# Kernel tuning notes

Measured on AMD Instinct MI355X. Metric: run time of the kernel, lower is better.

Reference implementation:

```python
import jax, jax.numpy as jnp
import numpy as np

NEG_SLOPE = 0.2

def gatv2(x, edge_index, Wl, bl, Wr, br, att, bias):
    # PyG GATv2Conv (share_weights=False, add_self_loops=True, concat=True)
    N = x.shape[0]
    H, D = att.shape
    src0, dst0 = edge_index[0], edge_index[1]
    # remove_self_loops + add_self_loops semantics: mask existing self loops,
    # append one self loop per node (keeps static shapes under jit)
    loop = jnp.arange(N, dtype=src0.dtype)
    src = jnp.concatenate([src0, loop])
    dst = jnp.concatenate([dst0, loop])
    keep = jnp.concatenate([src0 != dst0, jnp.ones(N, dtype=bool)])  # drop original i->i edges
    xl = (x @ Wl + bl).reshape(N, H, D)  # source-side transform
    xr = (x @ Wr + br).reshape(N, H, D)  # target-side transform
    e = xl[src] + xr[dst]                                  # [E,H,D]
    logits = jnp.einsum('ehd,hd->eh', jax.nn.leaky_relu(e, NEG_SLOPE), att)
    logits = jnp.where(keep[:, None], logits, -jnp.inf)
    m = jax.ops.segment_max(logits, dst, num_segments=N)   # [N,H]
    ex = jnp.where(keep[:, None], jnp.exp(logits - m[dst]), 0.0)
    denom = jax.ops.segment_sum(ex, dst, num_segments=N)   # [N,H]
    alpha = ex / (denom[dst] + 1e-16)                      # [E,H]
    out = jax.ops.segment_sum(alpha[..., None] * xl[src], dst, num_segments=N)
    return out.reshape(N, H * D) + bias

def setup_inputs() -> dict:
    key = jax.random.key(0)
    ks = jax.random.split(key, 20)
    N, E, F, Hd = 50000, 400000, 5, 128
    s = 0.05
    inp = {
        'x': jax.random.normal(ks[0], (N, F), dtype=jnp.float32),
        'edge_index': jax.random.randint(ks[1], (2, E), 0, N, dtype=jnp.int64),
        # node_embed MLP
        'W1': jax.random.normal(ks[2], (F, Hd), dtype=jnp.float32) * s,
        'b1': jnp.zeros((Hd,), jnp.float32),
        'W2': jax.random.normal(ks[3], (Hd, Hd), dtype=jnp.float32) * s,
        'b2': jnp.zeros((Hd,), jnp.float32),
        # gnn1: GATv2Conv(128 -> 128, heads=4)
        'Wl1': jax.random.normal(ks[4], (Hd, 4 * Hd), dtype=jnp.float32) * s,
        'bl1': jnp.zeros((4 * Hd,), jnp.float32),
        'Wr1': jax.random.normal(ks[5], (Hd, 4 * Hd), dtype=jnp.float32) * s,
        'br1': jnp.zeros((4 * Hd,), jnp.float32),
        'att1': jax.random.normal(ks[6], (4, Hd), dtype=jnp.float32) * s,
        'bias1': jnp.zeros((4 * Hd,), jnp.float32),
        # gnn2: GATv2Conv(512 -> 128, heads=1)
        'Wl2': jax.random.normal(ks[7], (4 * Hd, Hd), dtype=jnp.float32) * s,
        'bl2': jnp.zeros((Hd,), jnp.float32),
        'Wr2': jax.random.normal(ks[8], (4 * Hd, Hd), dtype=jnp.float32) * s,
        'br2': jnp.zeros((Hd,), jnp.float32),
        'att2': jax.random.normal(ks[9], (1, Hd), dtype=jnp.float32) * s,
        'bias2': jnp.zeros((Hd,), jnp.float32),
    }
    return inp

def reference(x, edge_index, W1, b1, W2, b2, Wl1, bl1, Wr1, br1, att1, bias1,
              Wl2, bl2, Wr2, br2, att2, bias2):
    h = jax.nn.relu(x @ W1 + b1) @ W2 + b2                 # node_embed MLP
    h = jax.nn.relu(gatv2(h, edge_index, Wl1, bl1, Wr1, br1, att1, bias1))
    out = gatv2(h, edge_index, Wl2, bl2, Wr2, br2, att2, bias2)
    return out  # [N, 128]
```

## Files before the change

### kernel.cpp

```cpp
#include <hip/hip_runtime.h>
#include <math.h>

typedef __attribute__((ext_vector_type(8))) short bf16x8;
typedef __attribute__((ext_vector_type(4))) float f32x4;
typedef unsigned short ushort;

static __device__ __forceinline__ ushort f2bf(float f) {
    unsigned u = __float_as_uint(f);
    u = u + 0x7fff + ((u >> 16) & 1);
    return (ushort)(u >> 16);
}
static __device__ __forceinline__ float bf2f(ushort h) {
    return __uint_as_float(((unsigned)h) << 16);
}


__global__ void k_init(int* __restrict__ counts, int N) {
    int i = blockIdx.x * blockDim.x + threadIdx.x;
    if (i < N) counts[i] = 1;
}

__global__ void k_count(const int* __restrict__ src, const int* __restrict__ dst,
                        int E, int* __restrict__ counts) {
    int e = blockIdx.x * blockDim.x + threadIdx.x;
    if (e < E) {
        int s = src[e], d = dst[e];
        if (s != d) atomicAdd(&counts[d], 1);
    }
}

__global__ __launch_bounds__(256) void k_blocksum(const int* __restrict__ counts, int N,
                                                  int* __restrict__ bsum) {
    __shared__ int s[256];
    int t = threadIdx.x, i = blockIdx.x * 256 + t;
    s[t] = (i < N) ? counts[i] : 0;
    __syncthreads();
    for (int off = 128; off > 0; off >>= 1) {
        if (t < off) s[t] += s[t + off];
        __syncthreads();
    }
    if (t == 0) bsum[blockIdx.x] = s[0];
}

__global__ __launch_bounds__(256) void k_scanblocks(const int* __restrict__ bsum, int NB,
                                                    int* __restrict__ boff,
                                                    int* __restrict__ rowptr, int N) {
    __shared__ int s[256];
    int t = threadIdx.x;
    int v = (t < NB) ? bsum[t] : 0;
    s[t] = v;
    __syncthreads();
    for (int off = 1; off < 256; off <<= 1) {
        int u = (t >= off) ? s[t - off] : 0;
        __syncthreads();
        s[t] += u;
        __syncthreads();
    }
    if (t < NB) boff[t] = s[t] - v;
    if (t == NB - 1) rowptr[N] = s[t];
}

__global__ __launch_bounds__(256) void k_scatter(const int* __restrict__ counts, int N,
                                                 const int* __restrict__ boff,
                                                 int* __restrict__ rowptr,
                                                 int* __restrict__ cursor) {
    __shared__ int s[256];
    int t = threadIdx.x, i = blockIdx.x * 256 + t;
    int c = (i < N) ? counts[i] : 0;
    s[t] = c;
    __syncthreads();
    for (int off = 1; off < 256; off <<= 1) {
        int u = (t >= off) ? s[t - off] : 0;
        __syncthreads();
        s[t] += u;
        __syncthreads();
    }
    if (i < N) {
        int excl = boff[blockIdx.x] + s[t] - c;
        rowptr[i] = excl;
        cursor[i] = excl;
    }
}

__global__ void k_fill(const int* __restrict__ src, const int* __restrict__ dst,
                       int E, int N, int* __restrict__ cursor, int* __restrict__ colA) {
    int i = blockIdx.x * blockDim.x + threadIdx.x;
    if (i < E) {
        int s = src[i], d = dst[i];
        if (s != d) { int p = atomicAdd(&cursor[d], 1); colA[p] = s; }
    } else if (i < E + N) {
        int n = i - E;
        int p = atomicAdd(&cursor[n], 1); colA[p] = n;
    }
}


__global__ __launch_bounds__(256) void k_repack(
    const float* __restrict__ W2, const float* __restrict__ Wl1,
    const float* __restrict__ Wr1, const float* __restrict__ Wl2,
    const float* __restrict__ Wr2,
    ushort* __restrict__ wfh, ushort* __restrict__ wfl)
{
    int job = blockIdx.y;
    int t = blockIdx.x * 256 + threadIdx.x;
    int ks = t >> 9, n = (t >> 6) & 7, l = t & 63;

    const float* W; int ldw, rowoff, col0;
    if (job == 0)      { W = W2;  ldw = 128; rowoff = 0;              col0 = 0; }
    else if (job < 5)  { W = Wl1; ldw = 512; rowoff = 0;              col0 = (job - 1) * 128; }
    else if (job < 9)  { W = Wr1; ldw = 512; rowoff = 0;              col0 = (job - 5) * 128; }
    else if (job < 13) { W = Wl2; ldw = 128; rowoff = (job - 9) * 128;  col0 = 0; }
    else               { W = Wr2; ldw = 128; rowoff = (job - 13) * 128; col0 = 0; }

    int krow = rowoff + ks * 32 + (l >> 4) * 8;
    int col = col0 + n * 16 + (l & 15);
    size_t dbase = (size_t)job * 16384 + (((size_t)(ks * 8 + n)) * 64 + l) * 8;
#pragma unroll
    for (int j = 0; j < 8; j++) {
        float v = W[(size_t)(krow + j) * ldw + col];
        ushort h = f2bf(v);
        ushort lo = f2bf(v - bf2f(h));
        wfh[dbase + j] = h;
        wfl[dbase + j] = lo;
    }
}


__global__ __launch_bounds__(256) void k_mlp1(
    const float* __restrict__ x, const float* __restrict__ W1, const float* __restrict__ b1,
    ushort* __restrict__ outh, ushort* __restrict__ outl, int N)
{
    int n = blockIdx.x * 2 + (threadIdx.x >> 7);
    int j = threadIdx.x & 127;
    if (n >= N) return;
    float s = b1[j];
#pragma unroll
    for (int k = 0; k < 5; k++) s = fmaf(x[(size_t)n * 5 + k], W1[k * 128 + j], s);
    s = fmaxf(s, 0.f);
    ushort h = f2bf(s);
    outh[(size_t)n * 128 + j] = h;
    outl[(size_t)n * 128 + j] = f2bf(s - bf2f(h));
}


__global__ __launch_bounds__(256) void gemm_mfma(
    const ushort* __restrict__ Ah, const ushort* __restrict__ Al,
    const ushort* __restrict__ wfh, const ushort* __restrict__ wfl,
    const float* __restrict__ bias,
    ushort* __restrict__ Ch, ushort* __restrict__ Cl,
    int M)
{
    int tid = threadIdx.x;
    int w = tid >> 6, l = tid & 63;
    int m0 = blockIdx.x * 128 + w * 32;
    int lr = l & 15, kg = l >> 4;

    f32x4 acc[2][8];
#pragma unroll
    for (int i = 0; i < 2; i++)
#pragma unroll
        for (int j = 0; j < 8; j++) acc[i][j] = (f32x4){0.f, 0.f, 0.f, 0.f};

    int row0 = m0 + lr, row1 = m0 + 16 + lr;
    bool ok0 = row0 < M, ok1 = row1 < M;
    const bf16x8 zz = {0, 0, 0, 0, 0, 0, 0, 0};

#pragma unroll
    for (int ks = 0; ks < 4; ks++) {
        int koff = ks * 32 + kg * 8;
        bf16x8 a0h = ok0 ? *(const bf16x8*)(Ah + (size_t)row0 * 128 + koff) : zz;
        bf16x8 a0l = ok0 ? *(const bf16x8*)(Al + (size_t)row0 * 128 + koff) : zz;
        bf16x8 a1h = ok1 ? *(const bf16x8*)(Ah + (size_t)row1 * 128 + koff) : zz;
        bf16x8 a1l = ok1 ? *(const bf16x8*)(Al + (size_t)row1 * 128 + koff) : zz;
#pragma unroll
        for (int n = 0; n < 8; n++) {
            size_t bo = (((size_t)(ks * 8 + n)) * 64 + l) * 8;
            bf16x8 bh = *(const bf16x8*)(wfh + bo);
            bf16x8 bl = *(const bf16x8*)(wfl + bo);
            acc[0][n] = __builtin_amdgcn_mfma_f32_16x16x32_bf16(a0h, bh, acc[0][n], 0, 0, 0);
            acc[0][n] = __builtin_amdgcn_mfma_f32_16x16x32_bf16(a0h, bl, acc[0][n], 0, 0, 0);
            acc[0][n] = __builtin_amdgcn_mfma_f32_16x16x32_bf16(a0l, bh, acc[0][n], 0, 0, 0);
            acc[1][n] = __builtin_amdgcn_mfma_f32_16x16x32_bf16(a1h, bh, acc[1][n], 0, 0, 0);
            acc[1][n] = __builtin_amdgcn_mfma_f32_16x16x32_bf16(a1h, bl, acc[1][n], 0, 0, 0);
            acc[1][n] = __builtin_amdgcn_mfma_f32_16x16x32_bf16(a1l, bh, acc[1][n], 0, 0, 0);
        }
    }

#pragma unroll
    for (int mf = 0; mf < 2; mf++) {
#pragma unroll
        for (int r = 0; r < 4; r++) {
            int row = m0 + mf * 16 + kg * 4 + r;
            if (row >= M) continue;
#pragma unroll
            for (int n = 0; n < 8; n++) {
                size_t idx = (size_t)row * 128 + n * 16 + lr;
                float v = acc[mf][n][r] + bias[n * 16 + lr];
                ushort h = f2bf(v);
                Ch[idx] = h;
                Cl[idx] = f2bf(v - bf2f(h));
            }
        }
    }
}


__global__ __launch_bounds__(256) void gemm_xlr1(
    const ushort* __restrict__ Ah, const ushort* __restrict__ Al,
    const ushort* __restrict__ wh, const ushort* __restrict__ wl,
    const float* __restrict__ bl1, const float* __restrict__ br1,
    ushort* __restrict__ out, int M)
{
    __shared__ __align__(16) ushort Bh[16384];
    __shared__ __align__(16) ushort Bl[16384];

    int tid = threadIdx.x;
    int w = tid >> 6, l = tid & 63;
    int m0 = blockIdx.x * 128 + w * 32;
    int lr = l & 15, kg = l >> 4;

    int row0 = m0 + lr, row1 = m0 + 16 + lr;
    bool ok0 = row0 < M, ok1 = row1 < M;
    const bf16x8 zz = {0, 0, 0, 0, 0, 0, 0, 0};

    bf16x8 a0h[4], a0l[4], a1h[4], a1l[4];
#pragma unroll
    for (int ks = 0; ks < 4; ks++) {
        int koff = ks * 32 + kg * 8;
        a0h[ks] = ok0 ? *(const bf16x8*)(Ah + (size_t)row0 * 128 + koff) : zz;
        a0l[ks] = ok0 ? *(const bf16x8*)(Al + (size_t)row0 * 128 + koff) : zz;
        a1h[ks] = ok1 ? *(const bf16x8*)(Ah + (size_t)row1 * 128 + koff) : zz;
        a1l[ks] = ok1 ? *(const bf16x8*)(Al + (size_t)row1 * 128 + koff) : zz;
    }

    for (int t = 0; t < 8; t++) {
        __syncthreads();
        {
            const float4* gh = (const float4*)(wh + (size_t)t * 16384);
            const float4* gl = (const float4*)(wl + (size_t)t * 16384);
            float4* sh = (float4*)Bh;
            float4* sl = (float4*)Bl;
#pragma unroll
            for (int i = 0; i < 8; i++) {
                sh[i * 256 + tid] = gh[i * 256 + tid];
                sl[i * 256 + tid] = gl[i * 256 + tid];
            }
        }
        __syncthreads();

        f32x4 acc[2][8];
#pragma unroll
        for (int i = 0; i < 2; i++)
#pragma unroll
            for (int j = 0; j < 8; j++) acc[i][j] = (f32x4){0.f, 0.f, 0.f, 0.f};

#pragma unroll
        for (int ks = 0; ks < 4; ks++) {
#pragma unroll
            for (int n = 0; n < 8; n++) {
                int bo = ((ks * 8 + n) * 64 + l) * 8;
                bf16x8 bh = *(const bf16x8*)(Bh + bo);
                bf16x8 bl = *(const bf16x8*)(Bl + bo);
                acc[0][n] = __builtin_amdgcn_mfma_f32_16x16x32_bf16(a0h[ks], bh, acc[0][n], 0, 0, 0);
                acc[0][n] = __builtin_amdgcn_mfma_f32_16x16x32_bf16(a0h[ks], bl, acc[0][n], 0, 0, 0);
                acc[0][n] = __builtin_amdgcn_mfma_f32_16x16x32_bf16(a0l[ks], bh, acc[0][n], 0, 0, 0);
                acc[1][n] = __builtin_amdgcn_mfma_f32_16x16x32_bf16(a1h[ks], bh, acc[1][n], 0, 0, 0);
                acc[1][n] = __builtin_amdgcn_mfma_f32_16x16x32_bf16(a1h[ks], bl, acc[1][n], 0, 0, 0);
                acc[1][n] = __builtin_amdgcn_mfma_f32_16x16x32_bf16(a1l[ks], bh, acc[1][n], 0, 0, 0);
            }
        }

        float bcol[8];
#pragma unroll
        for (int n = 0; n < 8; n++)
            bcol[n] = (t < 4) ? bl1[t * 128 + n * 16 + lr] : br1[(t - 4) * 128 + n * 16 + lr];

#pragma unroll
        for (int mf = 0; mf < 2; mf++) {
#pragma unroll
            for (int r = 0; r < 4; r++) {
                int row = m0 + mf * 16 + kg * 4 + r;
                if (row >= M) continue;
#pragma unroll
                for (int n = 0; n < 8; n++)
                    out[(size_t)row * 1024 + t * 128 + n * 16 + lr] = f2bf(acc[mf][n][r] + bcol[n]);
            }
        }
    }
}


__global__ __launch_bounds__(256) void gemm_xlr2(
    const ushort* __restrict__ A,
    const ushort* __restrict__ wfh, const ushort* __restrict__ wfl,
    const float* __restrict__ bl2, const float* __restrict__ br2,
    ushort* __restrict__ xl2, ushort* __restrict__ xr2, int M)
{
    __shared__ __align__(16) ushort Bh[16384];
    __shared__ __align__(16) ushort Bl[16384];

    int tid = threadIdx.x;
    int w = tid >> 6, l = tid & 63;
    int m0 = blockIdx.x * 64 + w * 16;
    int lr = l & 15, kg = l >> 4;

    int row0 = m0 + lr;
    bool ok0 = row0 < M;
    const bf16x8 zz = {0, 0, 0, 0, 0, 0, 0, 0};

    f32x4 acc[2][8];
#pragma unroll
    for (int i = 0; i < 2; i++)
#pragma unroll
        for (int j = 0; j < 8; j++) acc[i][j] = (f32x4){0.f, 0.f, 0.f, 0.f};

    for (int kc = 0; kc < 4; kc++) {
        bf16x8 ah[4];
#pragma unroll
        for (int ks = 0; ks < 4; ks++)
            ah[ks] = ok0 ? *(const bf16x8*)(A + (size_t)row0 * 512 + kc * 128 + ks * 32 + kg * 8) : zz;

        for (int t = 0; t < 2; t++) {
            int slot = 9 + t * 4 + kc;
            __syncthreads();
            {
                const float4* gh = (const float4*)(wfh + (size_t)slot * 16384);
                const float4* gl = (const float4*)(wfl + (size_t)slot * 16384);
                float4* sh = (float4*)Bh;
                float4* sl = (float4*)Bl;
#pragma unroll
                for (int i = 0; i < 8; i++) {
                    sh[i * 256 + tid] = gh[i * 256 + tid];
                    sl[i * 256 + tid] = gl[i * 256 + tid];
                }
            }
            __syncthreads();
#pragma unroll
            for (int ks = 0; ks < 4; ks++) {
#pragma unroll
                for (int n = 0; n < 8; n++) {
                    int bo = ((ks * 8 + n) * 64 + l) * 8;
                    bf16x8 bh = *(const bf16x8*)(Bh + bo);
                    bf16x8 bl = *(const bf16x8*)(Bl + bo);
                    acc[t][n] = __builtin_amdgcn_mfma_f32_16x16x32_bf16(ah[ks], bh, acc[t][n], 0, 0, 0);
                    acc[t][n] = __builtin_amdgcn_mfma_f32_16x16x32_bf16(ah[ks], bl, acc[t][n], 0, 0, 0);
                }
            }
        }
    }

#pragma unroll
    for (int r = 0; r < 4; r++) {
        int row = m0 + kg * 4 + r;
        if (row >= M) continue;
#pragma unroll
        for (int n = 0; n < 8; n++) {
            int col = n * 16 + lr;
            xl2[(size_t)row * 128 + col] = f2bf(acc[0][n][r] + bl2[col]);
            xr2[(size_t)row * 128 + col] = f2bf(acc[1][n][r] + br2[col]);
        }
    }
}


__global__ __launch_bounds__(256) void gat_edge4(
    const ushort* __restrict__ xlr,
    const float* __restrict__ att,
    const float* __restrict__ bias,
    const int* __restrict__ rowptr, const int* __restrict__ colA,
    ushort* __restrict__ h1,
    int N)
{
    int n = blockIdx.x;
    int h = threadIdx.x >> 6, l = threadIdx.x & 63;
    int g = l >> 4, q = l & 15;
    const bf16x8 zz = {0, 0, 0, 0, 0, 0, 0, 0};

    bf16x8 xrv = *(const bf16x8*)(xlr + (size_t)n * 1024 + (4 + h) * 128 + q * 8);
    float xr[8], at[8];
#pragma unroll
    for (int j = 0; j < 8; j++) {
        xr[j] = bf2f((ushort)xrv[j]);
        at[j] = att[h * 128 + q * 8 + j];
    }

    int k0 = rowptr[n], k1 = rowptr[n + 1];
    float m = -INFINITY, s = 0.f;
    float o[8];
#pragma unroll
    for (int j = 0; j < 8; j++) o[j] = 0.f;

    int k = k0 + g;
    bf16x8 vv = zz;
    if (k < k1) {
        int srcn = colA[k];
        vv = *(const bf16x8*)(xlr + (size_t)srcn * 1024 + h * 128 + q * 8);
    }
    for (; k < k1; k += 4) {
        bf16x8 nv = zz;
        if (k + 4 < k1) {
            int ns = colA[k + 4];
            nv = *(const bf16x8*)(xlr + (size_t)ns * 1024 + h * 128 + q * 8);
        }
        float v[8], c = 0.f;
#pragma unroll
        for (int j = 0; j < 8; j++) {
            v[j] = bf2f((ushort)vv[j]);
            float t = v[j] + xr[j];
            t = (t > 0.f) ? t : 0.2f * t;
            c = fmaf(t, at[j], c);
        }
        c += __shfl_xor(c, 1);
        c += __shfl_xor(c, 2);
        c += __shfl_xor(c, 4);
        c += __shfl_xor(c, 8);
        if (c > m) {
            float sc = __expf(m - c);
            s *= sc;
#pragma unroll
            for (int j = 0; j < 8; j++) o[j] *= sc;
            m = c;
        }
        float p = __expf(c - m);
        s += p;
#pragma unroll
        for (int j = 0; j < 8; j++) o[j] = fmaf(p, v[j], o[j]);
        vv = nv;
    }

#pragma unroll
    for (int off = 16; off <= 32; off <<= 1) {
        float m2 = __shfl_xor(m, off);
        float s2 = __shfl_xor(s, off);
        float o2[8];
#pragma unroll
        for (int j = 0; j < 8; j++) o2[j] = __shfl_xor(o[j], off);
        float nm = fmaxf(m, m2);
        float fa = (m > -INFINITY) ? __expf(m - nm) : 0.f;
        float fb = (m2 > -INFINITY) ? __expf(m2 - nm) : 0.f;
        s = s * fa + s2 * fb;
#pragma unroll
        for (int j = 0; j < 8; j++) o[j] = o[j] * fa + o2[j] * fb;
        m = nm;
    }

    if (g == 0) {
        float inv = 1.f / (s + 1e-16f);
        bf16x8 pk;
#pragma unroll
        for (int j = 0; j < 8; j++) {
            float r = fmaxf(o[j] * inv + bias[h * 128 + q * 8 + j], 0.f);
            pk[j] = (short)f2bf(r);
        }
        *(bf16x8*)(h1 + (size_t)n * 512 + h * 128 + q * 8) = pk;
    }
}


__global__ __launch_bounds__(256) void gat_edge1(
    const ushort* __restrict__ xl, const ushort* __restrict__ xr,
    const float* __restrict__ att, const float* __restrict__ bias,
    const int* __restrict__ rowptr, const int* __restrict__ colA,
    float* __restrict__ out, int N)
{
    int n = blockIdx.x * 4 + (threadIdx.x >> 6);
    if (n >= N) return;
    int l = threadIdx.x & 63;
    int g = l >> 4, q = l & 15;
    const bf16x8 zz = {0, 0, 0, 0, 0, 0, 0, 0};

    bf16x8 xrv = *(const bf16x8*)(xr + (size_t)n * 128 + q * 8);
    float xrr[8], at[8];
#pragma unroll
    for (int j = 0; j < 8; j++) {
        xrr[j] = bf2f((ushort)xrv[j]);
        at[j] = att[q * 8 + j];
    }

    int k0 = rowptr[n], k1 = rowptr[n + 1];
    float m = -INFINITY, s = 0.f;
    float o[8];
#pragma unroll
    for (int j = 0; j < 8; j++) o[j] = 0.f;

    int k = k0 + g;
    bf16x8 vv = zz;
    if (k < k1) {
        int srcn = colA[k];
        vv = *(const bf16x8*)(xl + (size_t)srcn * 128 + q * 8);
    }
    for (; k < k1; k += 4) {
        bf16x8 nv = zz;
        if (k + 4 < k1) {
            int ns = colA[k + 4];
            nv = *(const bf16x8*)(xl + (size_t)ns * 128 + q * 8);
        }
        float v[8], c = 0.f;
#pragma unroll
        for (int j = 0; j < 8; j++) {
            v[j] = bf2f((ushort)vv[j]);
            float t = v[j] + xrr[j];
            t = (t > 0.f) ? t : 0.2f * t;
            c = fmaf(t, at[j], c);
        }
        c += __shfl_xor(c, 1);
        c += __shfl_xor(c, 2);
        c += __shfl_xor(c, 4);
        c += __shfl_xor(c, 8);
        if (c > m) {
            float sc = __expf(m - c);
            s *= sc;
#pragma unroll
            for (int j = 0; j < 8; j++) o[j] *= sc;
            m = c;
        }
        float p = __expf(c - m);
        s += p;
#pragma unroll
        for (int j = 0; j < 8; j++) o[j] = fmaf(p, v[j], o[j]);
        vv = nv;
    }

#pragma unroll
    for (int off = 16; off <= 32; off <<= 1) {
        float m2 = __shfl_xor(m, off);
        float s2 = __shfl_xor(s, off);
        float o2[8];
#pragma unroll
        for (int j = 0; j < 8; j++) o2[j] = __shfl_xor(o[j], off);
        float nm = fmaxf(m, m2);
        float fa = (m > -INFINITY) ? __expf(m - nm) : 0.f;
        float fb = (m2 > -INFINITY) ? __expf(m2 - nm) : 0.f;
        s = s * fa + s2 * fb;
#pragma unroll
        for (int j = 0; j < 8; j++) o[j] = o[j] * fa + o2[j] * fb;
        m = nm;
    }

    if (g == 0) {
        float inv = 1.f / (s + 1e-16f);
        float4 r0, r1;
        float* p0 = (float*)&r0; float* p1 = (float*)&r1;
#pragma unroll
        for (int j = 0; j < 4; j++) {
            p0[j] = o[j] * inv + bias[q * 8 + j];
            p1[j] = o[j + 4] * inv + bias[q * 8 + j + 4];
        }
        *(float4*)(out + (size_t)n * 128 + q * 8)     = r0;
        *(float4*)(out + (size_t)n * 128 + q * 8 + 4) = r1;
    }
}


extern "C" void kernel_launch(void* const* d_in, const int* in_sizes, int n_in,
                              void* d_out, int out_size, void* d_ws, size_t ws_size,
                              hipStream_t stream) {
    const float* x    = (const float*)d_in[0];
    const int* ei     = (const int*)d_in[1];
    const float* W1   = (const float*)d_in[2];
    const float* b1   = (const float*)d_in[3];
    const float* W2   = (const float*)d_in[4];
    const float* b2   = (const float*)d_in[5];
    const float* Wl1  = (const float*)d_in[6];
    const float* bl1  = (const float*)d_in[7];
    const float* Wr1  = (const float*)d_in[8];
    const float* br1  = (const float*)d_in[9];
    const float* att1 = (const float*)d_in[10];
    const float* bias1= (const float*)d_in[11];
    const float* Wl2  = (const float*)d_in[12];
    const float* bl2  = (const float*)d_in[13];
    const float* Wr2  = (const float*)d_in[14];
    const float* br2  = (const float*)d_in[15];
    const float* att2 = (const float*)d_in[16];
    const float* bias2= (const float*)d_in[17];

    int E = in_sizes[1] / 2;
    int N = in_sizes[0] / 5;
    const int* srcE = ei;
    const int* dstE = ei + E;

    float* dout = (float*)d_out;

    ushort* xlr1 = (ushort*)d_ws;
    ushort* h1   = xlr1 + (size_t)N * 1024;
    ushort* h0h  = h1 + (size_t)N * 512;
    ushort* h0l  = h0h + (size_t)N * 128;
    ushort* wfh  = h0l + (size_t)N * 128;
    ushort* wfl  = wfh + 17 * 16384;
    int* rowptr = (int*)(wfl + 17 * 16384);
    int* cursor = rowptr + (N + 1);
    int* counts = cursor + N;
    int* colA   = counts + N;
    int* bsum   = colA + (E + N);
    int* boff   = bsum + 256;

    ushort* cCh = h1;
    ushort* cCl = h1 + (size_t)N * 128;
    ushort* xl2 = h0h;
    ushort* xr2 = h0l;

    int NB = (N + 255) / 256;

    k_init <<<(N + 255) / 256, 256, 0, stream>>>(counts, N);
    k_count<<<(E + 255) / 256, 256, 0, stream>>>(srcE, dstE, E, counts);
    k_blocksum <<<NB, 256, 0, stream>>>(counts, N, bsum);
    k_scanblocks<<<1, 256, 0, stream>>>(bsum, NB, boff, rowptr, N);
    k_scatter  <<<NB, 256, 0, stream>>>(counts, N, boff, rowptr, cursor);
    k_fill <<<(E + N + 255) / 256, 256, 0, stream>>>(srcE, dstE, E, N, cursor, colA);

    {
        dim3 g(8, 17);
        k_repack<<<g, 256, 0, stream>>>(W2, Wl1, Wr1, Wl2, Wr2, wfh, wfl);
    }

    int mb128 = (N + 127) / 128;
    int mb64  = (N + 63) / 64;

    k_mlp1<<<(N + 1) / 2, 256, 0, stream>>>(x, W1, b1, cCh, cCl, N);
    gemm_mfma<<<mb128, 256, 0, stream>>>(cCh, cCl, wfh, wfl, b2, h0h, h0l, N);

    gemm_xlr1<<<mb128, 256, 0, stream>>>(h0h, h0l, wfh + 16384, wfl + 16384,
                                         bl1, br1, xlr1, N);
    gat_edge4<<<N, 256, 0, stream>>>(xlr1, att1, bias1, rowptr, colA, h1, N);

    gemm_xlr2<<<mb64, 256, 0, stream>>>(h1, wfh, wfl, bl2, br2, xl2, xr2, N);
    gat_edge1<<<(N + 3) / 4, 256, 0, stream>>>(xl2, xr2, att2, bias2, rowptr, colA, dout, N);
}
```

Measured before the change: 386.0 us.

## Replace online softmax with self-loop reference max and packed f32 math in GAT edge kernels

New measurement: 391.8 us. About the same (+1.5%).

```diff
diff --git a/kernel.cpp b/kernel.cpp
--- a/kernel.cpp
+++ b/kernel.cpp
@@ -3,7 +3,9 @@
 
 typedef __attribute__((ext_vector_type(8))) short bf16x8;
 typedef __attribute__((ext_vector_type(4))) float f32x4;
+typedef __attribute__((ext_vector_type(2))) float f32x2;
 typedef unsigned short ushort;
+typedef unsigned int uint;
 
 static __device__ __forceinline__ ushort f2bf(float f) {
     unsigned u = __float_as_uint(f);
@@ -12,6 +14,17 @@
 }
 static __device__ __forceinline__ float bf2f(ushort h) {
     return __uint_as_float(((unsigned)h) << 16);
+}
+
+static __device__ __forceinline__ f32x2 pk_add(f32x2 a, f32x2 b) {
+    f32x2 d;
+    asm("v_pk_add_f32 %0, %1, %2" : "=v"(d) : "v"(a), "v"(b));
+    return d;
+}
+static __device__ __forceinline__ f32x2 pk_fma(f32x2 a, f32x2 b, f32x2 c) {
+    f32x2 d;
+    asm("v_pk_fma_f32 %0, %1, %2, %3" : "=v"(d) : "v"(a), "v"(b), "v"(c));
+    return d;
 }
 
 
@@ -377,18 +390,51 @@
     const bf16x8 zz = {0, 0, 0, 0, 0, 0, 0, 0};
 
     bf16x8 xrv = *(const bf16x8*)(xlr + (size_t)n * 1024 + (4 + h) * 128 + q * 8);
-    float xr[8], at[8];
-#pragma unroll
-    for (int j = 0; j < 8; j++) {
-        xr[j] = bf2f((ushort)xrv[j]);
-        at[j] = att[h * 128 + q * 8 + j];
-    }
+    f32x2 xr2[4], at6[4], at4[4];
+    {
+        const uint* xru = (const uint*)&xrv;
+#pragma unroll
+        for (int j = 0; j < 4; j++) {
+            xr2[j].x = __uint_as_float(xru[j] << 16);
+            xr2[j].y = __uint_as_float(xru[j] & 0xffff0000u);
+            float a0 = att[h * 128 + q * 8 + 2 * j];
+            float a1 = att[h * 128 + q * 8 + 2 * j + 1];
+            at6[j] = (f32x2){0.6f * a0, 0.6f * a1};
+            at4[j] = (f32x2){0.4f * a0, 0.4f * a1};
+        }
+    }
+
+    auto dotleaky = [&](bf16x8 vv, f32x2* v2o) -> float {
+        f32x2 c2 = (f32x2){0.f, 0.f};
+        const uint* vu = (const uint*)&vv;
+#pragma unroll
+        for (int j = 0; j < 4; j++) {
+            f32x2 v2;
+            v2.x = __uint_as_float(vu[j] << 16);
+            v2.y = __uint_as_float(vu[j] & 0xffff0000u);
+            f32x2 t2 = pk_add(v2, xr2[j]);
+            f32x2 a2 = (f32x2){fabsf(t2.x), fabsf(t2.y)};
+            c2 = pk_fma(t2, at6[j], c2);
+            c2 = pk_fma(a2, at4[j], c2);
+            v2o[j] = v2;
+        }
+        float c = c2.x + c2.y;
+        c += __shfl_xor(c, 1);
+        c += __shfl_xor(c, 2);
+        c += __shfl_xor(c, 4);
+        c += __shfl_xor(c, 8);
+        return c;
+    };
+
+    f32x2 tmp[4];
+    bf16x8 vself = *(const bf16x8*)(xlr + (size_t)n * 1024 + h * 128 + q * 8);
+    float c_self = dotleaky(vself, tmp);
 
     int k0 = rowptr[n], k1 = rowptr[n + 1];
-    float m = -INFINITY, s = 0.f;
-    float o[8];
-#pragma unroll
-    for (int j = 0; j < 8; j++) o[j] = 0.f;
+    float s = 0.f;
+    f32x2 o2[4];
+#pragma unroll
+    for (int j = 0; j < 4; j++) o2[j] = (f32x2){0.f, 0.f};
 
     int k = k0 + g;
     bf16x8 vv = zz;
@@ -402,55 +448,35 @@
             int ns = colA[k + 4];
             nv = *(const bf16x8*)(xlr + (size_t)ns * 1024 + h * 128 + q * 8);
         }
-        float v[8], c = 0.f;
-#pragma unroll
-        for (int j = 0; j < 8; j++) {
-            v[j] = bf2f((ushort)vv[j]);
-            float t = v[j] + xr[j];
-            t = (t > 0.f) ? t : 0.2f * t;
-            c = fmaf(t, at[j], c);
-        }
-        c += __shfl_xor(c, 1);
-        c += __shfl_xor(c, 2);
-        c += __shfl_xor(c, 4);
-        c += __shfl_xor(c, 8);
-        if (c > m) {
-            float sc = __expf(m - c);
-            s *= sc;
-#pragma unroll
-            for (int j = 0; j < 8; j++) o[j] *= sc;
-            m = c;
-        }
-        float p = __expf(c - m);
+        f32x2 v2[4];
+        float c = dotleaky(vv, v2);
+        float p = __expf(fminf(c - c_self, 80.f));
         s += p;
-#pragma unroll
-        for (int j = 0; j < 8; j++) o[j] = fmaf(p, v[j], o[j]);
+        f32x2 p2 = (f32x2){p, p};
+#pragma unroll
+        for (int j = 0; j < 4; j++) o2[j] = pk_fma(p2, v2[j], o2[j]);
         vv = nv;
     }
 
 #pragma unroll
     for (int off = 16; off <= 32; off <<= 1) {
-        float m2 = __shfl_xor(m, off);
-        float s2 = __shfl_xor(s, off);
-        float o2[8];
-#pragma unroll
-        for (int j = 0; j < 8; j++) o2[j] = __shfl_xor(o[j], off);
-        float nm = fmaxf(m, m2);
-        float fa = (m > -INFINITY) ? __expf(m - nm) : 0.f;
-        float fb = (m2 > -INFINITY) ? __expf(m2 - nm) : 0.f;
-        s = s * fa + s2 * fb;
-#pragma unroll
-        for (int j = 0; j < 8; j++) o[j] = o[j] * fa + o2[j] * fb;
-        m = nm;
+        s += __shfl_xor(s, off);
+#pragma unroll
+        for (int j = 0; j < 4; j++) {
+            o2[j].x += __shfl_xor(o2[j].x, off);
+            o2[j].y += __shfl_xor(o2[j].y, off);
+        }
     }
 
     if (g == 0) {
         float inv = 1.f / (s + 1e-16f);
         bf16x8 pk;
 #pragma unroll
-        for (int j = 0; j < 8; j++) {
-            float r = fmaxf(o[j] * inv + bias[h * 128 + q * 8 + j], 0.f);
-            pk[j] = (short)f2bf(r);
+        for (int j = 0; j < 4; j++) {
+            float r0 = fmaxf(o2[j].x * inv + bias[h * 128 + q * 8 + 2 * j], 0.f);
+            float r1 = fmaxf(o2[j].y * inv + bias[h * 128 + q * 8 + 2 * j + 1], 0.f);
+            pk[2 * j] = (short)f2bf(r0);
+            pk[2 * j + 1] = (short)f2bf(r1);
         }
         *(bf16x8*)(h1 + (size_t)n * 512 + h * 128 + q * 8) = pk;
     }
@@ -470,18 +496,51 @@
     const bf16x8 zz = {0, 0, 0, 0, 0, 0, 0, 0};
 
     bf16x8 xrv = *(const bf16x8*)(xr + (size_t)n * 128 + q * 8);
-    float xrr[8], at[8];
-#pragma unroll
-    for (int j = 0; j < 8; j++) {
-        xrr[j] = bf2f((ushort)xrv[j]);
-        at[j] = att[q * 8 + j];
-    }
+    f32x2 xr2[4], at6[4], at4[4];
+    {
+        const uint* xru = (const uint*)&xrv;
+#pragma unroll
+        for (int j = 0; j < 4; j++) {
+            xr2[j].x = __uint_as_float(xru[j] << 16);
+            xr2[j].y = __uint_as_float(xru[j] & 0xffff0000u);
+            float a0 = att[q * 8 + 2 * j];
+            float a1 = att[q * 8 + 2 * j + 1];
+            at6[j] = (f32x2){0.6f * a0, 0.6f * a1};
+            at4[j] = (f32x2){0.4f * a0, 0.4f * a1};
+        }
+    }
+
+    auto dotleaky = [&](bf16x8 vv, f32x2* v2o) -> float {
+        f32x2 c2 = (f32x2){0.f, 0.f};
+        const uint* vu = (const uint*)&vv;
+#pragma unroll
+        for (int j = 0; j < 4; j++) {
+            f32x2 v2;
+            v2.x = __uint_as_float(vu[j] << 16);
+            v2.y = __uint_as_float(vu[j] & 0xffff0000u);
+            f32x2 t2 = pk_add(v2, xr2[j]);
+            f32x2 a2 = (f32x2){fabsf(t2.x), fabsf(t2.y)};
+            c2 = pk_fma(t2, at6[j], c2);
+            c2 = pk_fma(a2, at4[j], c2);
+            v2o[j] = v2;
+        }
+        float c = c2.x + c2.y;
+        c += __shfl_xor(c, 1);
+        c += __shfl_xor(c, 2);
+        c += __shfl_xor(c, 4);
+        c += __shfl_xor(c, 8);
+        return c;
+    };
+
+    f32x2 tmp[4];
+    bf16x8 vself = *(const bf16x8*)(xl + (size_t)n * 128 + q * 8);
+    float c_self = dotleaky(vself, tmp);
 
     int k0 = rowptr[n], k1 = rowptr[n + 1];
-    float m = -INFINITY, s = 0.f;
-    float o[8];
-#pragma unroll
-    for (int j = 0; j < 8; j++) o[j] = 0.f;
+    float s = 0.f;
+    f32x2 o2[4];
+#pragma unroll
+    for (int j = 0; j < 4; j++) o2[j] = (f32x2){0.f, 0.f};
 
     int k = k0 + g;
     bf16x8 vv = zz;
@@ -495,57 +554,37 @@
             int ns = colA[k + 4];
             nv = *(const bf16x8*)(xl + (size_t)ns * 128 + q * 8);
         }
-        float v[8], c = 0.f;
-#pragma unroll
-        for (int j = 0; j < 8; j++) {
-            v[j] = bf2f((ushort)vv[j]);
-            float t = v[j] + xrr[j];
-            t = (t > 0.f) ? t : 0.2f * t;
-            c = fmaf(t, at[j], c);
-        }
-        c += __shfl_xor(c, 1);
-        c += __shfl_xor(c, 2);
-        c += __shfl_xor(c, 4);
-        c += __shfl_xor(c, 8);
-        if (c > m) {
-            float sc = __expf(m - c);
-            s *= sc;
-#pragma unroll
-            for (int j = 0; j < 8; j++) o[j] *= sc;
-            m = c;
-        }
-        float p = __expf(c - m);
+        f32x2 v2[4];
+        float c = dotleaky(vv, v2);
+        float p = __expf(fminf(c - c_self, 80.f));
         s += p;
-#pragma unroll
-        for (int j = 0; j < 8; j++) o[j] = fmaf(p, v[j], o[j]);
+        f32x2 p2 = (f32x2){p, p};
+#pragma unroll
+        for (int j = 0; j < 4; j++) o2[j] = pk_fma(p2, v2[j], o2[j]);
         vv = nv;
     }
 
 #pragma unroll
     for (int off = 16; off <= 32; off <<= 1) {
-        float m2 = __shfl_xor(m, off);
-        float s2 = __shfl_xor(s, off);
-        float o2[8];
-#pragma unroll
-        for (int j = 0; j < 8; j++) o2[j] = __shfl_xor(o[j], off);
-        float nm = fmaxf(m, m2);
-        float fa = (m > -INFINITY) ? __expf(m - nm) : 0.f;
-        float fb = (m2 > -INFINITY) ? __expf(m2 - nm) : 0.f;
-        s = s * fa + s2 * fb;
-#pragma unroll
-        for (int j = 0; j < 8; j++) o[j] = o[j] * fa + o2[j] * fb;
-        m = nm;
+        s += __shfl_xor(s, off);
+#pragma unroll
+        for (int j = 0; j < 4; j++) {
+            o2[j].x += __shfl_xor(o2[j].x, off);
+            o2[j].y += __shfl_xor(o2[j].y, off);
+        }
     }
 
     if (g == 0) {
         float inv = 1.f / (s + 1e-16f);
         float4 r0, r1;
-        float* p0 = (float*)&r0; float* p1 = (float*)&r1;
-#pragma unroll
-        for (int j = 0; j < 4; j++) {
-            p0[j] = o[j] * inv + bias[q * 8 + j];
-            p1[j] = o[j + 4] * inv + bias[q * 8 + j + 4];
-        }
+        r0.x = o2[0].x * inv + bias[q * 8 + 0];
+        r0.y = o2[0].y * inv + bias[q * 8 + 1];
+        r0.z = o2[1].x * inv + bias[q * 8 + 2];
+        r0.w = o2[1].y * inv + bias[q * 8 + 3];
+        r1.x = o2[2].x * inv + bias[q * 8 + 4];
+        r1.y = o2[2].y * inv + bias[q * 8 + 5];
+        r1.z = o2[3].x * inv + bias[q * 8 + 6];
+        r1.w = o2[3].y * inv + bias[q * 8 + 7];
         *(float4*)(out + (size_t)n * 128 + q * 8)     = r0;
         *(float4*)(out + (size_t)n * 128 + q * 8 + 4) = r1;
     }
```
